# Kernel optimization log

Hardware: AMD Instinct MI355X
Metric: run time of the kernel (lower is better)

The kernel has to match this reference:

```python
import jax, jax.numpy as jnp
import numpy as np

B_, S_, D_, N_, R_ = 2, 2048, 1024, 16, 64  # batch, seq, d_model, d_state, dt_rank


def setup_inputs() -> dict:
    key = jax.random.key(0)
    ks = jax.random.split(key, 12)
    x = jax.random.normal(ks[0], (B_, S_, D_), dtype=jnp.float32)
    # params (xavier-ish scale)
    W_dtw = jax.random.normal(ks[1], (R_, D_), dtype=jnp.float32) * (1.0 / np.sqrt(D_))
    W_dt = jax.random.normal(ks[2], (D_, R_), dtype=jnp.float32) * (1.0 / np.sqrt(R_))
    b_dt = jnp.zeros((D_,), dtype=jnp.float32)
    A_log = jnp.log(jax.random.uniform(ks[3], (D_, N_), minval=0.5, maxval=1.5, dtype=jnp.float32))
    W_B = jax.random.normal(ks[4], (N_, D_), dtype=jnp.float32) * (1.0 / np.sqrt(D_))
    W_C = jax.random.normal(ks[5], (N_, D_), dtype=jnp.float32) * (1.0 / np.sqrt(D_))
    Dp = jnp.ones((D_,), dtype=jnp.float32)
    ln_g = jnp.ones((D_,), dtype=jnp.float32)
    ln_b = jnp.zeros((D_,), dtype=jnp.float32)
    W_out = jax.random.normal(ks[6], (D_, D_), dtype=jnp.float32) * (1.0 / np.sqrt(D_))
    return {"x": x, "W_dtw": W_dtw, "W_dt": W_dt, "b_dt": b_dt, "A_log": A_log,
            "W_B": W_B, "W_C": W_C, "Dp": Dp, "ln_g": ln_g, "ln_b": ln_b, "W_out": W_out}


def _layernorm(y, g, b, eps=1e-5):
    mu = jnp.mean(y, axis=-1, keepdims=True)
    var = jnp.mean(jnp.square(y - mu), axis=-1, keepdims=True)
    return (y - mu) * jax.lax.rsqrt(var + eps) * g + b


def reference(x, W_dtw, W_dt, b_dt, A_log, W_B, W_C, Dp, ln_g, ln_b, W_out):
    # projections
    dt = jnp.einsum('bsd,rd->bsr', x, W_dtw)                 # [B,S,R]
    delta = jax.nn.softplus(jnp.einsum('bsr,dr->bsd', dt, W_dt) + b_dt)  # [B,S,D]
    Bm = jnp.einsum('bsd,nd->bsn', x, W_B)                   # [B,S,N]
    Cm = jnp.einsum('bsd,nd->bsn', x, W_C)                   # [B,S,N]
    A = -jnp.exp(A_log)                                      # [D,N]

    def step(h, inp):
        d_t, b_t, c_t, x_t = inp                             # [B,D],[B,N],[B,N],[B,D]
        dA = jnp.exp(d_t[..., None] * A)                     # [B,D,N]
        h = dA * h + (d_t[..., None] * b_t[:, None, :]) * x_t[..., None]
        y_t = jnp.sum(h * c_t[:, None, :], axis=-1)          # [B,D]
        return h, y_t

    h0 = jnp.zeros((x.shape[0], x.shape[2], A.shape[1]), dtype=x.dtype)
    xs = (jnp.swapaxes(delta, 0, 1), jnp.swapaxes(Bm, 0, 1),
          jnp.swapaxes(Cm, 0, 1), jnp.swapaxes(x, 0, 1))
    _, ys = jax.lax.scan(step, h0, xs)                       # ys: [S,B,D]
    y = jnp.swapaxes(ys, 0, 1) + Dp * x                      # [B,S,D]
    y = _layernorm(y, ln_g, ln_b)
    return jnp.einsum('bsd,ed->bse', y, W_out)
```

## Files before the change

### kernel.cpp

```cpp
#include <hip/hip_runtime.h>
#include <hip/hip_bf16.h>

#define B_ 2
#define S_ 2048
#define D_ 1024
#define N_ 16
#define R_ 64
#define NC 64
#define CL 32
#define BS_ (B_*S_)
#define KSPLIT 8

typedef __attribute__((ext_vector_type(4))) float f32x4;
typedef __attribute__((ext_vector_type(8))) short bf16x8;
typedef __attribute__((ext_vector_type(8))) unsigned short u16x8;

__device__ __forceinline__ unsigned short f2b(float v) {
  unsigned u = __builtin_bit_cast(unsigned, v);
  unsigned r = ((u >> 16) & 1u) + 0x7FFFu;
  return (unsigned short)((u + r) >> 16);
}

__device__ __forceinline__ void gload_lds16(const void* g, void* l) {
  __builtin_amdgcn_global_load_lds(
      (const __attribute__((address_space(1))) unsigned int*)g,
      (__attribute__((address_space(3))) unsigned int*)l, 16, 0, 0);
}

__global__ __launch_bounds__(256) void k_castall(
    const float* __restrict__ W_dtw, const float* __restrict__ W_B,
    const float* __restrict__ W_C, const float* __restrict__ W_dt,
    const float* __restrict__ W_out,
    unsigned short* __restrict__ Wcat, unsigned short* __restrict__ wdtb,
    unsigned short* __restrict__ wob) {
  int i = (blockIdx.x * 256 + threadIdx.x) * 4;
  const float* s; unsigned short* d; int off;
  if (i < 65536)       { s = W_dtw; d = Wcat;         off = 0; }
  else if (i < 81920)  { s = W_B;   d = Wcat + 65536; off = 65536; }
  else if (i < 98304)  { s = W_C;   d = Wcat + 81920; off = 81920; }
  else if (i < 163840) { s = W_dt;  d = wdtb;         off = 98304; }
  else                 { s = W_out; d = wob;          off = 163840; }
  int j = i - off;
  float4 v = *(const float4*)&s[j];
  ushort4 o;
  o.x = f2b(v.x); o.y = f2b(v.y); o.z = f2b(v.z); o.w = f2b(v.w);
  *(ushort4*)&d[j] = o;
}

__global__ __launch_bounds__(256, 2) void k_proj(
    const float* __restrict__ x, const unsigned short* __restrict__ Wcat,
    float* __restrict__ part) {
  __shared__ __align__(16) unsigned short Xs[2][64 * 64];
  __shared__ __align__(16) unsigned short Ws[2][96 * 64];
  const int tid = threadIdx.x;
  const int lane = tid & 63, w = tid >> 6;
  const size_t row0 = (size_t)blockIdx.x * 64;
  const int kbase = blockIdx.y * (D_ / KSPLIT);
  f32x4 acc[6] = {};

  auto stage = [&](int buf, int k0) {
    #pragma unroll
    for (int i = 0; i < 2; ++i) {
      int id = i * 256 + tid; int row = id >> 3, s = id & 7;
      const float* gp = &x[(row0 + row) * D_ + k0 + s * 8];
      float4 v0 = *(const float4*)gp;
      float4 v1 = *(const float4*)(gp + 4);
      u16x8 u;
      u[0] = f2b(v0.x); u[1] = f2b(v0.y); u[2] = f2b(v0.z); u[3] = f2b(v0.w);
      u[4] = f2b(v1.x); u[5] = f2b(v1.y); u[6] = f2b(v1.z); u[7] = f2b(v1.w);
      *(u16x8*)&Xs[buf][row * 64 + ((s ^ (row & 7)) << 3)] = u;
    }
    #pragma unroll
    for (int i = 0; i < 3; ++i) {
      int id = i * 256 + tid; int row = id >> 3, s = id & 7;
      gload_lds16(Wcat + (size_t)row * D_ + k0 + ((s ^ (row & 7)) << 3),
                  Ws[buf] + row * 64 + s * 8);
    }
  };
  stage(0, kbase);
  __syncthreads();
  int cur = 0;
  const int r = lane & 15, kg = lane >> 4;
  for (int t = 0; t < 2; ++t) {
    if (t < 1) stage(cur ^ 1, kbase + 64);
    #pragma unroll
    for (int ks = 0; ks < 2; ++ks) {
      const int arow = w * 16 + r;
      bf16x8 a = *(const bf16x8*)&Xs[cur][arow * 64 + ((((ks << 2) | kg) ^ (arow & 7)) << 3)];
      #pragma unroll
      for (int nt = 0; nt < 6; ++nt) {
        const int brow = nt * 16 + r;
        bf16x8 b = *(const bf16x8*)&Ws[cur][brow * 64 + ((((ks << 2) | kg) ^ (brow & 7)) << 3)];
        acc[nt] = __builtin_amdgcn_mfma_f32_16x16x32_bf16(a, b, acc[nt], 0, 0, 0);
      }
    }
    __syncthreads();
    cur ^= 1;
  }
  const int cr = lane >> 4, cc = lane & 15;
  float* pb = part + (size_t)blockIdx.y * (BS_ * 96);
  #pragma unroll
  for (int nt = 0; nt < 6; ++nt)
    #pragma unroll
    for (int j = 0; j < 4; ++j)
      pb[(row0 + w * 16 + cr * 4 + j) * 96 + nt * 16 + cc] = acc[nt][j];
}

__global__ __launch_bounds__(256) void k_projred(
    const float* __restrict__ part, unsigned short* __restrict__ dtb,
    float* __restrict__ Bm, float* __restrict__ Cm) {
  int e = blockIdx.x * 256 + threadIdx.x;
  int row = e / 96, col = e - row * 96;
  float s = 0.f;
  #pragma unroll
  for (int p = 0; p < KSPLIT; ++p) s += part[e + (size_t)p * (BS_ * 96)];
  if (col < 64)      dtb[row * R_ + col] = f2b(s);
  else if (col < 80) Bm[row * N_ + col - 64] = s;
  else               Cm[row * N_ + col - 80] = s;
}

__global__ __launch_bounds__(256) void k_delta(
    const unsigned short* __restrict__ dtb, const unsigned short* __restrict__ wdtb,
    const float* __restrict__ b_dt, float* __restrict__ delta) {
  __shared__ __align__(16) unsigned short As[128 * 64];
  __shared__ __align__(16) unsigned short Bs[128 * 64];
  const int tid = threadIdx.x;
  const int lane = tid & 63, wid = tid >> 6;
  const int wr = wid >> 1, wc = wid & 1;
  const size_t row0 = (size_t)blockIdx.x * 128;
  const size_t col0 = (size_t)blockIdx.y * 128;
  f32x4 acc[4][4] = {};

  {
    const int r = tid >> 3, s = tid & 7;
    #pragma unroll
    for (int i = 0; i < 4; ++i) {
      const int row = i * 32 + r;
      const int gs = s ^ (row & 7);
      gload_lds16(dtb + (row0 + row) * R_ + gs * 8, As + row * 64 + s * 8);
      gload_lds16(wdtb + (col0 + row) * R_ + gs * 8, Bs + row * 64 + s * 8);
    }
  }
  __syncthreads();
  const int r = lane & 15, kg = lane >> 4;
  #pragma unroll
  for (int ks = 0; ks < 2; ++ks) {
    bf16x8 a[4], b[4];
    #pragma unroll
    for (int m = 0; m < 4; ++m) {
      const int arow = wr * 64 + m * 16 + r;
      a[m] = *(const bf16x8*)&As[arow * 64 + (((ks << 2) | kg) ^ (arow & 7)) * 8];
    }
    #pragma unroll
    for (int n = 0; n < 4; ++n) {
      const int brow = wc * 64 + n * 16 + r;
      b[n] = *(const bf16x8*)&Bs[brow * 64 + (((ks << 2) | kg) ^ (brow & 7)) * 8];
    }
    #pragma unroll
    for (int m = 0; m < 4; ++m)
      #pragma unroll
      for (int n = 0; n < 4; ++n)
        acc[m][n] = __builtin_amdgcn_mfma_f32_16x16x32_bf16(a[m], b[n], acc[m][n], 0, 0, 0);
  }
  const int cr = lane >> 4, cc = lane & 15;
  #pragma unroll
  for (int m = 0; m < 4; ++m) {
    #pragma unroll
    for (int n = 0; n < 4; ++n) {
      const int d = (int)col0 + wc * 64 + n * 16 + cc;
      const float bd = b_dt[d];
      #pragma unroll
      for (int j = 0; j < 4; ++j) {
        size_t trow = row0 + wr * 64 + m * 16 + cr * 4 + j;
        float v = acc[m][n][j] + bd;
        float sp = fmaxf(v, 0.f) + log1pf(__expf(-fabsf(v)));
        delta[trow * D_ + d] = sp;
      }
    }
  }
}

__global__ __launch_bounds__(256) void k_scan1(
    const float* __restrict__ x, const float* __restrict__ delta,
    const float* __restrict__ Bm, const float* __restrict__ A_log,
    float* __restrict__ aprod, float* __restrict__ hend) {
  __shared__ __align__(16) float sd[CL][64];
  __shared__ __align__(16) float sx[CL][64];
  __shared__ __align__(16) float sB[CL][N_];
  const int tid = threadIdx.x;
  const int db = blockIdx.x & 15;
  const int c  = (blockIdx.x >> 4) & (NC - 1);
  const int b  = blockIdx.x >> 10;
  const int d0 = db * 64;
  const size_t tokbase = (size_t)(b * S_ + c * CL);

  {
    int s = tid >> 4, jf = (tid & 15) * 4;
    size_t g = (tokbase + s) * D_ + d0 + jf;
    gload_lds16(&delta[g], &sd[s][jf]);
    gload_lds16(&x[g],     &sx[s][jf]);
    gload_lds16(&delta[g + (size_t)16 * D_], &sd[s + 16][jf]);
    gload_lds16(&x[g + (size_t)16 * D_],     &sx[s + 16][jf]);
    if (tid < 128) {
      int s2 = tid >> 2, nf = (tid & 3) * 4;
      gload_lds16(&Bm[(tokbase + s2) * N_ + nf], &sB[s2][nf]);
    }
  }
  const int nq = tid & 3, dl = tid >> 2;
  const int d = d0 + dl;
  float4 av = *(const float4*)&A_log[(size_t)d * N_ + nq * 4];
  float Ad0 = -__expf(av.x), Ad1 = -__expf(av.y);
  float Ad2 = -__expf(av.z), Ad3 = -__expf(av.w);
  __syncthreads();

  float ap0 = 1.f, ap1 = 1.f, ap2 = 1.f, ap3 = 1.f;
  float h0 = 0.f, h1 = 0.f, h2 = 0.f, h3 = 0.f;
  #pragma unroll 8
  for (int s = 0; s < CL; ++s) {
    float dlt = sd[s][dl];
    float dbx = dlt * sx[s][dl];
    float4 Bv = *(const float4*)&sB[s][nq * 4];
    float da0 = __expf(dlt * Ad0), da1 = __expf(dlt * Ad1);
    float da2 = __expf(dlt * Ad2), da3 = __expf(dlt * Ad3);
    ap0 *= da0; ap1 *= da1; ap2 *= da2; ap3 *= da3;
    h0 = da0 * h0 + dbx * Bv.x;
    h1 = da1 * h1 + dbx * Bv.y;
    h2 = da2 * h2 + dbx * Bv.z;
    h3 = da3 * h3 + dbx * Bv.w;
  }
  size_t o = (((size_t)(b * NC + c)) * D_ + d) * N_ + nq * 4;
  *(float4*)&aprod[o] = make_float4(ap0, ap1, ap2, ap3);
  *(float4*)&hend[o]  = make_float4(h0, h1, h2, h3);
}

__global__ __launch_bounds__(256) void k_scan2(
    const float* __restrict__ aprod, const float* __restrict__ hend,
    float* __restrict__ hstart) {
  int g = blockIdx.x * 256 + threadIdx.x;
  int n = g & (N_ - 1);
  int d = (g >> 4) & (D_ - 1);
  int b = g >> 14;
  float h = 0.f;
  for (int c = 0; c < NC; ++c) {
    size_t idx = (((size_t)b * NC + c) * D_ + d) * N_ + n;
    hstart[idx] = h;
    h = aprod[idx] * h + hend[idx];
  }
}

__global__ __launch_bounds__(256) void k_scan3(
    const float* __restrict__ x, const float* __restrict__ delta,
    const float* __restrict__ Bm, const float* __restrict__ Cm,
    const float* __restrict__ A_log, const float* __restrict__ hstart,
    const float* __restrict__ Dp, float* __restrict__ ypre) {
  __shared__ __align__(16) float sd[CL][64];
  __shared__ __align__(16) float sx[CL][64];
  __shared__ __align__(16) float sB[CL][N_];
  __shared__ __align__(16) float sC[CL][N_];
  __shared__ __align__(16) float sy[CL][64];
  const int tid = threadIdx.x;
  const int db = blockIdx.x & 15;
  const int c  = (blockIdx.x >> 4) & (NC - 1);
  const int b  = blockIdx.x >> 10;
  const int d0 = db * 64;
  const size_t tokbase = (size_t)(b * S_ + c * CL);

  {
    int s = tid >> 4, jf = (tid & 15) * 4;
    size_t g = (tokbase + s) * D_ + d0 + jf;
    gload_lds16(&delta[g], &sd[s][jf]);
    gload_lds16(&x[g],     &sx[s][jf]);
    gload_lds16(&delta[g + (size_t)16 * D_], &sd[s + 16][jf]);
    gload_lds16(&x[g + (size_t)16 * D_],     &sx[s + 16][jf]);
    if (tid < 128) {
      int s2 = tid >> 2, nf = (tid & 3) * 4;
      gload_lds16(&Bm[(tokbase + s2) * N_ + nf], &sB[s2][nf]);
      gload_lds16(&Cm[(tokbase + s2) * N_ + nf], &sC[s2][nf]);
    }
  }
  const int nq = tid & 3, dl = tid >> 2;
  const int d = d0 + dl;
  float4 av = *(const float4*)&A_log[(size_t)d * N_ + nq * 4];
  float Ad0 = -__expf(av.x), Ad1 = -__expf(av.y);
  float Ad2 = -__expf(av.z), Ad3 = -__expf(av.w);
  float h0, h1, h2, h3;
  {
    size_t o = (((size_t)(b * NC + c)) * D_ + d) * N_ + nq * 4;
    float4 v = *(const float4*)&hstart[o];
    h0 = v.x; h1 = v.y; h2 = v.z; h3 = v.w;
  }
  const float Dpd = Dp[d];
  __syncthreads();

  #pragma unroll 8
  for (int s = 0; s < CL; ++s) {
    float dlt = sd[s][dl];
    float xv  = sx[s][dl];
    float dbx = dlt * xv;
    float4 Bv = *(const float4*)&sB[s][nq * 4];
    float4 Cv = *(const float4*)&sC[s][nq * 4];
    float da0 = __expf(dlt * Ad0), da1 = __expf(dlt * Ad1);
    float da2 = __expf(dlt * Ad2), da3 = __expf(dlt * Ad3);
    h0 = da0 * h0 + dbx * Bv.x;
    h1 = da1 * h1 + dbx * Bv.y;
    h2 = da2 * h2 + dbx * Bv.z;
    h3 = da3 * h3 + dbx * Bv.w;
    float y = h0 * Cv.x + h1 * Cv.y + h2 * Cv.z + h3 * Cv.w;
    y += __shfl_xor(y, 1);
    y += __shfl_xor(y, 2);
    if (nq == 0) sy[s][dl] = y + Dpd * xv;
  }
  __syncthreads();
  {
    int s = tid >> 3, j = (tid & 7) * 8;
    size_t g = (tokbase + s) * D_ + d0 + j;
    *(float4*)&ypre[g]     = *(float4*)&sy[s][j];
    *(float4*)&ypre[g + 4] = *(float4*)&sy[s][j + 4];
  }
}

__device__ __forceinline__ float block_sum256(float v, float* sm) {
  #pragma unroll
  for (int o = 32; o > 0; o >>= 1) v += __shfl_down(v, o, 64);
  int w = threadIdx.x >> 6;
  __syncthreads();
  if ((threadIdx.x & 63) == 0) sm[w] = v;
  __syncthreads();
  return (sm[0] + sm[1]) + (sm[2] + sm[3]);
}

__global__ __launch_bounds__(256) void k_ln(
    const float* __restrict__ ypre, const float* __restrict__ g,
    const float* __restrict__ bta, unsigned short* __restrict__ ybf) {
  __shared__ float sm[4];
  const int t = blockIdx.x;
  const int tid = threadIdx.x;
  size_t base = (size_t)t * D_ + tid * 4;
  float4 v = *(const float4*)&ypre[base];
  float s1 = block_sum256(v.x + v.y + v.z + v.w, sm);
  float mu = s1 * (1.f / D_);
  float cx = v.x - mu, cy = v.y - mu, cz = v.z - mu, cw = v.w - mu;
  float s2 = block_sum256(cx*cx + cy*cy + cz*cz + cw*cw, sm);
  float rs = rsqrtf(s2 * (1.f / D_) + 1e-5f);
  float4 gg = *(const float4*)&g[tid * 4];
  float4 bb = *(const float4*)&bta[tid * 4];
  ushort4 o;
  o.x = f2b(cx * rs * gg.x + bb.x);
  o.y = f2b(cy * rs * gg.y + bb.y);
  o.z = f2b(cz * rs * gg.z + bb.z);
  o.w = f2b(cw * rs * gg.w + bb.w);
  *(ushort4*)&ybf[base] = o;
}

__device__ __forceinline__ void stage128x64(const unsigned short* __restrict__ g,
                                            size_t row0, int k0,
                                            unsigned short* lds, int tid) {
  const int r = tid >> 3, s = tid & 7;
  #pragma unroll
  for (int i = 0; i < 4; ++i) {
    const int row = i * 32 + r;
    const int gs = s ^ (row & 7);
    gload_lds16(g + ((row0 + row) << 10) + k0 + (gs << 3), lds + row * 64 + s * 8);
  }
}

__device__ __forceinline__ void stage64x64(const unsigned short* __restrict__ g,
                                           size_t row0, int k0,
                                           unsigned short* lds, int tid) {
  const int r = tid >> 3, s = tid & 7;
  #pragma unroll
  for (int i = 0; i < 2; ++i) {
    const int row = i * 32 + r;
    const int gs = s ^ (row & 7);
    gload_lds16(g + ((row0 + row) << 10) + k0 + (gs << 3), lds + row * 64 + s * 8);
  }
}

__global__ __launch_bounds__(256, 2) void k_out(const unsigned short* __restrict__ Y,
                                                const unsigned short* __restrict__ W,
                                                float* __restrict__ O) {
  __shared__ __align__(16) unsigned short As[2][128 * 64];
  __shared__ __align__(16) unsigned short Bs[2][64 * 64];
  const int tid = threadIdx.x;
  const int lane = tid & 63, wid = tid >> 6;
  const size_t row0 = (size_t)blockIdx.x * 128;
  const size_t col0 = (size_t)blockIdx.y * 64;
  f32x4 acc[2][4] = {};

  stage128x64(Y, row0, 0, As[0], tid);
  stage64x64(W, col0, 0, Bs[0], tid);
  __syncthreads();

  int cur = 0;
  const int r = lane & 15, kg = lane >> 4;
  for (int t = 0; t < 16; ++t) {
    if (t + 1 < 16) {
      stage128x64(Y, row0, (t + 1) * 64, As[cur ^ 1], tid);
      stage64x64(W, col0, (t + 1) * 64, Bs[cur ^ 1], tid);
    }
    #pragma unroll
    for (int ks = 0; ks < 2; ++ks) {
      bf16x8 a[2], b[4];
      #pragma unroll
      for (int m = 0; m < 2; ++m) {
        const int arow = wid * 32 + m * 16 + r;
        a[m] = *(const bf16x8*)&As[cur][arow * 64 + (((ks << 2) | kg) ^ (arow & 7)) * 8];
      }
      #pragma unroll
      for (int n = 0; n < 4; ++n) {
        const int brow = n * 16 + r;
        b[n] = *(const bf16x8*)&Bs[cur][brow * 64 + (((ks << 2) | kg) ^ (brow & 7)) * 8];
      }
      #pragma unroll
      for (int m = 0; m < 2; ++m)
        #pragma unroll
        for (int n = 0; n < 4; ++n)
          acc[m][n] = __builtin_amdgcn_mfma_f32_16x16x32_bf16(a[m], b[n], acc[m][n], 0, 0, 0);
    }
    __syncthreads();
    cur ^= 1;
  }

  const int cr = lane >> 4, cc = lane & 15;
  #pragma unroll
  for (int m = 0; m < 2; ++m) {
    #pragma unroll
    for (int n = 0; n < 4; ++n) {
      size_t orow = row0 + wid * 32 + m * 16 + cr * 4;
      float* op = O + orow * D_ + col0 + n * 16 + cc;
      #pragma unroll
      for (int j = 0; j < 4; ++j) op[(size_t)j * D_] = acc[m][n][j];
    }
  }
}

extern "C" void kernel_launch(void* const* d_in, const int* in_sizes, int n_in,
                              void* d_out, int out_size, void* d_ws, size_t ws_size,
                              hipStream_t stream) {
  const float* x     = (const float*)d_in[0];
  const float* W_dtw = (const float*)d_in[1];
  const float* W_dt  = (const float*)d_in[2];
  const float* b_dt  = (const float*)d_in[3];
  const float* A_log = (const float*)d_in[4];
  const float* W_B   = (const float*)d_in[5];
  const float* W_C   = (const float*)d_in[6];
  const float* Dp    = (const float*)d_in[7];
  const float* ln_g  = (const float*)d_in[8];
  const float* ln_b  = (const float*)d_in[9];
  const float* W_out = (const float*)d_in[10];
  float* out = (float*)d_out;

  float* ws = (float*)d_ws;
  float* delta  = ws;
  float* ypre   = delta  + (size_t)BS_ * D_;
  float* Bm     = ypre   + (size_t)BS_ * D_;
  float* Cm     = Bm     + (size_t)BS_ * N_;
  float* aprod  = Cm     + (size_t)BS_ * N_;
  float* hend   = aprod  + (size_t)B_ * NC * D_ * N_;
  float* hstart = hend   + (size_t)B_ * NC * D_ * N_;
  float* part   = hstart + (size_t)B_ * NC * D_ * N_;
  unsigned short* Wcat = (unsigned short*)(part + (size_t)KSPLIT * BS_ * 96);
  unsigned short* wdtb = Wcat + (size_t)96 * D_;
  unsigned short* wob  = wdtb + (size_t)D_ * R_;
  unsigned short* ybf  = wob  + (size_t)D_ * D_;
  unsigned short* dtb  = ybf  + (size_t)BS_ * D_;

  k_castall<<<dim3(1184), dim3(256), 0, stream>>>(W_dtw, W_B, W_C, W_dt, W_out,
                                                  Wcat, wdtb, wob);
  k_proj<<<dim3(BS_ / 64, KSPLIT), dim3(256), 0, stream>>>(x, Wcat, part);
  k_projred<<<dim3(BS_ * 96 / 256), dim3(256), 0, stream>>>(part, dtb, Bm, Cm);
  k_delta<<<dim3(BS_ / 128, D_ / 128), dim3(256), 0, stream>>>(dtb, wdtb, b_dt, delta);
  k_scan1<<<dim3(B_ * NC * (D_ / 64)), dim3(256), 0, stream>>>(x, delta, Bm, A_log,
                                                               aprod, hend);
  k_scan2<<<dim3(B_ * D_ * N_ / 256), dim3(256), 0, stream>>>(aprod, hend, hstart);
  k_scan3<<<dim3(B_ * NC * (D_ / 64)), dim3(256), 0, stream>>>(x, delta, Bm, Cm,
                                                               A_log, hstart, Dp, ypre);
  k_ln<<<dim3(BS_), dim3(256), 0, stream>>>(ypre, ln_g, ln_b, ybf);
  k_out<<<dim3(BS_ / 128, D_ / 64), dim3(256), 0, stream>>>(ybf, wob, out);
}
```

Measured before the change: 110.6 us.

## Fold dt low-rank projection into a dense effective weight and derive chunk decay from delta sums

Precomputes W_eff = W_dt·W_dtw (1024x1024, bf16) so delta is computed with a single dense GEMM from x, fused with the B/C projection in one kernel. This replaces the split-K projection, its reduction kernel and the second small GEMM, at the cost of a larger dense GEMM (K=1024, N=1024 instead of rank 64) and an extra bf16 rounding of the fused weight. The scan also stops storing per-chunk products of decays and instead stores the per-channel sum of delta, recomputing the decay as exp(A·sum) in the carry pass. That cuts aprod memory traffic by a factor of N.

```diff
diff --git a/kernel.cpp b/kernel.cpp
--- a/kernel.cpp
+++ b/kernel.cpp
@@ -9,7 +9,6 @@
 #define NC 64
 #define CL 32
 #define BS_ (B_*S_)
-#define KSPLIT 8
 
 typedef __attribute__((ext_vector_type(4))) float f32x4;
 typedef __attribute__((ext_vector_type(8))) short bf16x8;
@@ -28,39 +27,103 @@
 }
 
 __global__ __launch_bounds__(256) void k_castall(
-    const float* __restrict__ W_dtw, const float* __restrict__ W_B,
-    const float* __restrict__ W_C, const float* __restrict__ W_dt,
-    const float* __restrict__ W_out,
-    unsigned short* __restrict__ Wcat, unsigned short* __restrict__ wdtb,
-    unsigned short* __restrict__ wob) {
+    const float* __restrict__ W_B, const float* __restrict__ W_C,
+    const float* __restrict__ W_dt, const float* __restrict__ W_out,
+    const float* __restrict__ W_dtw,
+    unsigned short* __restrict__ WBC, unsigned short* __restrict__ wdtb,
+    unsigned short* __restrict__ wob, unsigned short* __restrict__ wdtwT) {
   int i = (blockIdx.x * 256 + threadIdx.x) * 4;
-  const float* s; unsigned short* d; int off;
-  if (i < 65536)       { s = W_dtw; d = Wcat;         off = 0; }
-  else if (i < 81920)  { s = W_B;   d = Wcat + 65536; off = 65536; }
-  else if (i < 98304)  { s = W_C;   d = Wcat + 81920; off = 81920; }
-  else if (i < 163840) { s = W_dt;  d = wdtb;         off = 98304; }
-  else                 { s = W_out; d = wob;          off = 163840; }
-  int j = i - off;
-  float4 v = *(const float4*)&s[j];
-  ushort4 o;
-  o.x = f2b(v.x); o.y = f2b(v.y); o.z = f2b(v.z); o.w = f2b(v.w);
-  *(ushort4*)&d[j] = o;
-}
-
-__global__ __launch_bounds__(256, 2) void k_proj(
-    const float* __restrict__ x, const unsigned short* __restrict__ Wcat,
-    float* __restrict__ part) {
-  __shared__ __align__(16) unsigned short Xs[2][64 * 64];
-  __shared__ __align__(16) unsigned short Ws[2][96 * 64];
+  if (i < 1146880) {
+    const float* s; unsigned short* d; int off;
+    if (i < 16384)      { s = W_B;   d = WBC;         off = 0; }
+    else if (i < 32768) { s = W_C;   d = WBC + 16384; off = 16384; }
+    else if (i < 98304) { s = W_dt;  d = wdtb;        off = 32768; }
+    else                { s = W_out; d = wob;         off = 98304; }
+    int j = i - off;
+    float4 v = *(const float4*)&s[j];
+    ushort4 o;
+    o.x = f2b(v.x); o.y = f2b(v.y); o.z = f2b(v.z); o.w = f2b(v.w);
+    *(ushort4*)&d[j] = o;
+  } else {
+    int j = i - 1146880;
+    int r = j >> 10, e = j & 1023;
+    float4 v = *(const float4*)&W_dtw[j];
+    wdtwT[(size_t)(e + 0) * 64 + r] = f2b(v.x);
+    wdtwT[(size_t)(e + 1) * 64 + r] = f2b(v.y);
+    wdtwT[(size_t)(e + 2) * 64 + r] = f2b(v.z);
+    wdtwT[(size_t)(e + 3) * 64 + r] = f2b(v.w);
+  }
+}
+
+__global__ __launch_bounds__(256) void k_weff(
+    const unsigned short* __restrict__ wdtb, const unsigned short* __restrict__ wdtwT,
+    unsigned short* __restrict__ weff) {
+  __shared__ __align__(16) unsigned short As[128 * 64];
+  __shared__ __align__(16) unsigned short Bs[128 * 64];
   const int tid = threadIdx.x;
-  const int lane = tid & 63, w = tid >> 6;
-  const size_t row0 = (size_t)blockIdx.x * 64;
-  const int kbase = blockIdx.y * (D_ / KSPLIT);
-  f32x4 acc[6] = {};
-
-  auto stage = [&](int buf, int k0) {
-    #pragma unroll
-    for (int i = 0; i < 2; ++i) {
+  const int lane = tid & 63, wid = tid >> 6;
+  const int wr = wid >> 1, wc = wid & 1;
+  const size_t row0 = (size_t)blockIdx.x * 128;
+  const size_t col0 = (size_t)blockIdx.y * 128;
+  f32x4 acc[4][4] = {};
+  {
+    const int r = tid >> 3, s = tid & 7;
+    #pragma unroll
+    for (int i = 0; i < 4; ++i) {
+      const int row = i * 32 + r;
+      const int gs = s ^ (row & 7);
+      gload_lds16(wdtb + (row0 + row) * R_ + gs * 8, As + row * 64 + s * 8);
+      gload_lds16(wdtwT + (col0 + row) * R_ + gs * 8, Bs + row * 64 + s * 8);
+    }
+  }
+  __syncthreads();
+  const int r = lane & 15, kg = lane >> 4;
+  #pragma unroll
+  for (int ks = 0; ks < 2; ++ks) {
+    bf16x8 a[4], b[4];
+    #pragma unroll
+    for (int m = 0; m < 4; ++m) {
+      const int arow = wr * 64 + m * 16 + r;
+      a[m] = *(const bf16x8*)&As[arow * 64 + (((ks << 2) | kg) ^ (arow & 7)) * 8];
+    }
+    #pragma unroll
+    for (int n = 0; n < 4; ++n) {
+      const int brow = wc * 64 + n * 16 + r;
+      b[n] = *(const bf16x8*)&Bs[brow * 64 + (((ks << 2) | kg) ^ (brow & 7)) * 8];
+    }
+    #pragma unroll
+    for (int m = 0; m < 4; ++m)
+      #pragma unroll
+      for (int n = 0; n < 4; ++n)
+        acc[m][n] = __builtin_amdgcn_mfma_f32_16x16x32_bf16(a[m], b[n], acc[m][n], 0, 0, 0);
+  }
+  const int cr = lane >> 4, cc = lane & 15;
+  #pragma unroll
+  for (int m = 0; m < 4; ++m)
+    #pragma unroll
+    for (int n = 0; n < 4; ++n)
+      #pragma unroll
+      for (int j = 0; j < 4; ++j)
+        weff[(row0 + wr * 64 + m * 16 + cr * 4 + j) * D_ + col0 + wc * 64 + n * 16 + cc]
+            = f2b(acc[m][n][j]);
+}
+
+__global__ __launch_bounds__(256, 2) void k_deltaBC(
+    const float* __restrict__ x, const unsigned short* __restrict__ weff,
+    const unsigned short* __restrict__ WBC, const float* __restrict__ b_dt,
+    float* __restrict__ delta, float* __restrict__ Bm, float* __restrict__ Cm) {
+  __shared__ __align__(16) unsigned short Xs[2][128 * 64];
+  __shared__ __align__(16) unsigned short Bs[2][128 * 64];
+  const int tid = threadIdx.x;
+  const int lane = tid & 63, wid = tid >> 6;
+  const size_t row0 = (size_t)blockIdx.x * 128;
+  const int by = blockIdx.y;
+  const bool bc = (by == 8);
+  f32x4 acc[4][4] = {};
+
+  auto stageX = [&](int buf, int k0) {
+    #pragma unroll
+    for (int i = 0; i < 4; ++i) {
       int id = i * 256 + tid; int row = id >> 3, s = id & 7;
       const float* gp = &x[(row0 + row) * D_ + k0 + s * 8];
       float4 v0 = *(const float4*)gp;
@@ -70,111 +133,107 @@
       u[4] = f2b(v1.x); u[5] = f2b(v1.y); u[6] = f2b(v1.z); u[7] = f2b(v1.w);
       *(u16x8*)&Xs[buf][row * 64 + ((s ^ (row & 7)) << 3)] = u;
     }
-    #pragma unroll
-    for (int i = 0; i < 3; ++i) {
-      int id = i * 256 + tid; int row = id >> 3, s = id & 7;
-      gload_lds16(Wcat + (size_t)row * D_ + k0 + ((s ^ (row & 7)) << 3),
-                  Ws[buf] + row * 64 + s * 8);
-    }
   };
-  stage(0, kbase);
+  auto stageB = [&](int buf, int k0) {
+    if (!bc) {
+      const size_t c0 = (size_t)by * 128;
+      const int r = tid >> 3, s = tid & 7;
+      #pragma unroll
+      for (int i = 0; i < 4; ++i) {
+        const int row = i * 32 + r;
+        const int gs = s ^ (row & 7);
+        gload_lds16(weff + (c0 + row) * D_ + k0 + (gs << 3), Bs[buf] + row * 64 + s * 8);
+      }
+    } else {
+      const int row = tid >> 3, s = tid & 7;
+      const int gs = s ^ (row & 7);
+      gload_lds16(WBC + (size_t)row * D_ + k0 + (gs << 3), Bs[buf] + row * 64 + s * 8);
+    }
+  };
+
+  stageX(0, 0); stageB(0, 0);
   __syncthreads();
   int cur = 0;
   const int r = lane & 15, kg = lane >> 4;
-  for (int t = 0; t < 2; ++t) {
-    if (t < 1) stage(cur ^ 1, kbase + 64);
-    #pragma unroll
-    for (int ks = 0; ks < 2; ++ks) {
-      const int arow = w * 16 + r;
-      bf16x8 a = *(const bf16x8*)&Xs[cur][arow * 64 + ((((ks << 2) | kg) ^ (arow & 7)) << 3)];
-      #pragma unroll
-      for (int nt = 0; nt < 6; ++nt) {
-        const int brow = nt * 16 + r;
-        bf16x8 b = *(const bf16x8*)&Ws[cur][brow * 64 + ((((ks << 2) | kg) ^ (brow & 7)) << 3)];
-        acc[nt] = __builtin_amdgcn_mfma_f32_16x16x32_bf16(a, b, acc[nt], 0, 0, 0);
+  for (int t = 0; t < 16; ++t) {
+    if (t + 1 < 16) { stageX(cur ^ 1, (t + 1) * 64); stageB(cur ^ 1, (t + 1) * 64); }
+    if (!bc) {
+      const int wr = wid >> 1, wc = wid & 1;
+      #pragma unroll
+      for (int ks = 0; ks < 2; ++ks) {
+        bf16x8 a[4], b[4];
+        #pragma unroll
+        for (int m = 0; m < 4; ++m) {
+          const int arow = wr * 64 + m * 16 + r;
+          a[m] = *(const bf16x8*)&Xs[cur][arow * 64 + (((ks << 2) | kg) ^ (arow & 7)) * 8];
+        }
+        #pragma unroll
+        for (int n = 0; n < 4; ++n) {
+          const int brow = wc * 64 + n * 16 + r;
+          b[n] = *(const bf16x8*)&Bs[cur][brow * 64 + (((ks << 2) | kg) ^ (brow & 7)) * 8];
+        }
+        #pragma unroll
+        for (int m = 0; m < 4; ++m)
+          #pragma unroll
+          for (int n = 0; n < 4; ++n)
+            acc[m][n] = __builtin_amdgcn_mfma_f32_16x16x32_bf16(a[m], b[n], acc[m][n], 0, 0, 0);
+      }
+    } else {
+      #pragma unroll
+      for (int ks = 0; ks < 2; ++ks) {
+        bf16x8 a[2], b[2];
+        #pragma unroll
+        for (int m = 0; m < 2; ++m) {
+          const int arow = wid * 32 + m * 16 + r;
+          a[m] = *(const bf16x8*)&Xs[cur][arow * 64 + (((ks << 2) | kg) ^ (arow & 7)) * 8];
+        }
+        #pragma unroll
+        for (int n = 0; n < 2; ++n) {
+          const int brow = n * 16 + r;
+          b[n] = *(const bf16x8*)&Bs[cur][brow * 64 + (((ks << 2) | kg) ^ (brow & 7)) * 8];
+        }
+        #pragma unroll
+        for (int m = 0; m < 2; ++m)
+          #pragma unroll
+          for (int n = 0; n < 2; ++n)
+            acc[m][n] = __builtin_amdgcn_mfma_f32_16x16x32_bf16(a[m], b[n], acc[m][n], 0, 0, 0);
       }
     }
     __syncthreads();
     cur ^= 1;
   }
+
   const int cr = lane >> 4, cc = lane & 15;
-  float* pb = part + (size_t)blockIdx.y * (BS_ * 96);
-  #pragma unroll
-  for (int nt = 0; nt < 6; ++nt)
-    #pragma unroll
-    for (int j = 0; j < 4; ++j)
-      pb[(row0 + w * 16 + cr * 4 + j) * 96 + nt * 16 + cc] = acc[nt][j];
-}
-
-__global__ __launch_bounds__(256) void k_projred(
-    const float* __restrict__ part, unsigned short* __restrict__ dtb,
-    float* __restrict__ Bm, float* __restrict__ Cm) {
-  int e = blockIdx.x * 256 + threadIdx.x;
-  int row = e / 96, col = e - row * 96;
-  float s = 0.f;
-  #pragma unroll
-  for (int p = 0; p < KSPLIT; ++p) s += part[e + (size_t)p * (BS_ * 96)];
-  if (col < 64)      dtb[row * R_ + col] = f2b(s);
-  else if (col < 80) Bm[row * N_ + col - 64] = s;
-  else               Cm[row * N_ + col - 80] = s;
-}
-
-__global__ __launch_bounds__(256) void k_delta(
-    const unsigned short* __restrict__ dtb, const unsigned short* __restrict__ wdtb,
-    const float* __restrict__ b_dt, float* __restrict__ delta) {
-  __shared__ __align__(16) unsigned short As[128 * 64];
-  __shared__ __align__(16) unsigned short Bs[128 * 64];
-  const int tid = threadIdx.x;
-  const int lane = tid & 63, wid = tid >> 6;
-  const int wr = wid >> 1, wc = wid & 1;
-  const size_t row0 = (size_t)blockIdx.x * 128;
-  const size_t col0 = (size_t)blockIdx.y * 128;
-  f32x4 acc[4][4] = {};
-
-  {
-    const int r = tid >> 3, s = tid & 7;
-    #pragma unroll
-    for (int i = 0; i < 4; ++i) {
-      const int row = i * 32 + r;
-      const int gs = s ^ (row & 7);
-      gload_lds16(dtb + (row0 + row) * R_ + gs * 8, As + row * 64 + s * 8);
-      gload_lds16(wdtb + (col0 + row) * R_ + gs * 8, Bs + row * 64 + s * 8);
-    }
-  }
-  __syncthreads();
-  const int r = lane & 15, kg = lane >> 4;
-  #pragma unroll
-  for (int ks = 0; ks < 2; ++ks) {
-    bf16x8 a[4], b[4];
+  if (!bc) {
+    const int wr = wid >> 1, wc = wid & 1;
     #pragma unroll
     for (int m = 0; m < 4; ++m) {
-      const int arow = wr * 64 + m * 16 + r;
-      a[m] = *(const bf16x8*)&As[arow * 64 + (((ks << 2) | kg) ^ (arow & 7)) * 8];
-    }
-    #pragma unroll
-    for (int n = 0; n < 4; ++n) {
-      const int brow = wc * 64 + n * 16 + r;
-      b[n] = *(const bf16x8*)&Bs[brow * 64 + (((ks << 2) | kg) ^ (brow & 7)) * 8];
-    }
-    #pragma unroll
-    for (int m = 0; m < 4; ++m)
-      #pragma unroll
-      for (int n = 0; n < 4; ++n)
-        acc[m][n] = __builtin_amdgcn_mfma_f32_16x16x32_bf16(a[m], b[n], acc[m][n], 0, 0, 0);
-  }
-  const int cr = lane >> 4, cc = lane & 15;
-  #pragma unroll
-  for (int m = 0; m < 4; ++m) {
-    #pragma unroll
-    for (int n = 0; n < 4; ++n) {
-      const int d = (int)col0 + wc * 64 + n * 16 + cc;
-      const float bd = b_dt[d];
-      #pragma unroll
-      for (int j = 0; j < 4; ++j) {
-        size_t trow = row0 + wr * 64 + m * 16 + cr * 4 + j;
-        float v = acc[m][n][j] + bd;
-        float sp = fmaxf(v, 0.f) + log1pf(__expf(-fabsf(v)));
-        delta[trow * D_ + d] = sp;
+      #pragma unroll
+      for (int n = 0; n < 4; ++n) {
+        const int d = by * 128 + wc * 64 + n * 16 + cc;
+        const float bd = b_dt[d];
+        #pragma unroll
+        for (int j = 0; j < 4; ++j) {
+          size_t trow = row0 + wr * 64 + m * 16 + cr * 4 + j;
+          float v = acc[m][n][j] + bd;
+          float sp = fmaxf(v, 0.f) + log1pf(__expf(-fabsf(v)));
+          delta[trow * D_ + d] = sp;
+        }
+      }
+    }
+  } else {
+    #pragma unroll
+    for (int m = 0; m < 2; ++m) {
+      #pragma unroll
+      for (int n = 0; n < 2; ++n) {
+        const int col = n * 16 + cc;
+        #pragma unroll
+        for (int j = 0; j < 4; ++j) {
+          size_t trow = row0 + wid * 32 + m * 16 + cr * 4 + j;
+          float v = acc[m][n][j];
+          if (col < 16) Bm[trow * N_ + col] = v;
+          else          Cm[trow * N_ + col - 16] = v;
+        }
       }
     }
   }
@@ -183,7 +242,7 @@
 __global__ __launch_bounds__(256) void k_scan1(
     const float* __restrict__ x, const float* __restrict__ delta,
     const float* __restrict__ Bm, const float* __restrict__ A_log,
-    float* __restrict__ aprod, float* __restrict__ hend) {
+    float* __restrict__ sdsum, float* __restrict__ hend) {
   __shared__ __align__(16) float sd[CL][64];
   __shared__ __align__(16) float sx[CL][64];
   __shared__ __align__(16) float sB[CL][N_];
@@ -213,38 +272,40 @@
   float Ad2 = -__expf(av.z), Ad3 = -__expf(av.w);
   __syncthreads();
 
-  float ap0 = 1.f, ap1 = 1.f, ap2 = 1.f, ap3 = 1.f;
+  float sds = 0.f;
   float h0 = 0.f, h1 = 0.f, h2 = 0.f, h3 = 0.f;
   #pragma unroll 8
   for (int s = 0; s < CL; ++s) {
     float dlt = sd[s][dl];
     float dbx = dlt * sx[s][dl];
+    sds += dlt;
     float4 Bv = *(const float4*)&sB[s][nq * 4];
     float da0 = __expf(dlt * Ad0), da1 = __expf(dlt * Ad1);
     float da2 = __expf(dlt * Ad2), da3 = __expf(dlt * Ad3);
-    ap0 *= da0; ap1 *= da1; ap2 *= da2; ap3 *= da3;
     h0 = da0 * h0 + dbx * Bv.x;
     h1 = da1 * h1 + dbx * Bv.y;
     h2 = da2 * h2 + dbx * Bv.z;
     h3 = da3 * h3 + dbx * Bv.w;
   }
   size_t o = (((size_t)(b * NC + c)) * D_ + d) * N_ + nq * 4;
-  *(float4*)&aprod[o] = make_float4(ap0, ap1, ap2, ap3);
-  *(float4*)&hend[o]  = make_float4(h0, h1, h2, h3);
+  *(float4*)&hend[o] = make_float4(h0, h1, h2, h3);
+  if (nq == 0) sdsum[(size_t)(b * NC + c) * D_ + d] = sds;
 }
 
 __global__ __launch_bounds__(256) void k_scan2(
-    const float* __restrict__ aprod, const float* __restrict__ hend,
-    float* __restrict__ hstart) {
+    const float* __restrict__ sdsum, const float* __restrict__ hend,
+    const float* __restrict__ A_log, float* __restrict__ hstart) {
   int g = blockIdx.x * 256 + threadIdx.x;
   int n = g & (N_ - 1);
   int d = (g >> 4) & (D_ - 1);
   int b = g >> 14;
+  float Ad = -__expf(A_log[(size_t)d * N_ + n]);
   float h = 0.f;
   for (int c = 0; c < NC; ++c) {
     size_t idx = (((size_t)b * NC + c) * D_ + d) * N_ + n;
+    float ap = __expf(Ad * sdsum[(size_t)(b * NC + c) * D_ + d]);
     hstart[idx] = h;
-    h = aprod[idx] * h + hend[idx];
+    h = ap * h + hend[idx];
   }
 }
 
@@ -455,24 +516,24 @@
   float* ypre   = delta  + (size_t)BS_ * D_;
   float* Bm     = ypre   + (size_t)BS_ * D_;
   float* Cm     = Bm     + (size_t)BS_ * N_;
-  float* aprod  = Cm     + (size_t)BS_ * N_;
-  float* hend   = aprod  + (size_t)B_ * NC * D_ * N_;
+  float* hend   = Cm     + (size_t)BS_ * N_;
   float* hstart = hend   + (size_t)B_ * NC * D_ * N_;
-  float* part   = hstart + (size_t)B_ * NC * D_ * N_;
-  unsigned short* Wcat = (unsigned short*)(part + (size_t)KSPLIT * BS_ * 96);
-  unsigned short* wdtb = Wcat + (size_t)96 * D_;
-  unsigned short* wob  = wdtb + (size_t)D_ * R_;
-  unsigned short* ybf  = wob  + (size_t)D_ * D_;
-  unsigned short* dtb  = ybf  + (size_t)BS_ * D_;
-
-  k_castall<<<dim3(1184), dim3(256), 0, stream>>>(W_dtw, W_B, W_C, W_dt, W_out,
-                                                  Wcat, wdtb, wob);
-  k_proj<<<dim3(BS_ / 64, KSPLIT), dim3(256), 0, stream>>>(x, Wcat, part);
-  k_projred<<<dim3(BS_ * 96 / 256), dim3(256), 0, stream>>>(part, dtb, Bm, Cm);
-  k_delta<<<dim3(BS_ / 128, D_ / 128), dim3(256), 0, stream>>>(dtb, wdtb, b_dt, delta);
+  float* sdsum  = hstart + (size_t)B_ * NC * D_ * N_;
+  unsigned short* WBC   = (unsigned short*)(sdsum + (size_t)B_ * NC * D_);
+  unsigned short* wdtb  = WBC   + (size_t)32 * D_;
+  unsigned short* wdtwT = wdtb  + (size_t)D_ * R_;
+  unsigned short* weff  = wdtwT + (size_t)D_ * R_;
+  unsigned short* wob   = weff  + (size_t)D_ * D_;
+  unsigned short* ybf   = wob   + (size_t)D_ * D_;
+
+  k_castall<<<dim3(1184), dim3(256), 0, stream>>>(W_B, W_C, W_dt, W_out, W_dtw,
+                                                  WBC, wdtb, wob, wdtwT);
+  k_weff<<<dim3(8, 8), dim3(256), 0, stream>>>(wdtb, wdtwT, weff);
+  k_deltaBC<<<dim3(BS_ / 128, 9), dim3(256), 0, stream>>>(x, weff, WBC, b_dt,
+                                                          delta, Bm, Cm);
   k_scan1<<<dim3(B_ * NC * (D_ / 64)), dim3(256), 0, stream>>>(x, delta, Bm, A_log,
-                                                               aprod, hend);
-  k_scan2<<<dim3(B_ * D_ * N_ / 256), dim3(256), 0, stream>>>(aprod, hend, hstart);
+                                                               sdsum, hend);
+  k_scan2<<<dim3(B_ * D_ * N_ / 256), dim3(256), 0, stream>>>(sdsum, hend, A_log, hstart);
   k_scan3<<<dim3(B_ * NC * (D_ / 64)), dim3(256), 0, stream>>>(x, delta, Bm, Cm,
                                                                A_log, hstart, Dp, ypre);
   k_ln<<<dim3(BS_), dim3(256), 0, stream>>>(ypre, ln_g, ln_b, ybf);
```

After: 124.7 us. +12.7%, slower.
